# Kernel tuning notes

Measured on AMD Instinct MI355X. Metric: run time of the kernel, lower is better.

## Reference

```python
import jax, jax.numpy as jnp
import numpy as np

B, S, E, H = 8, 2048, 1024, 64  # batch, seq (== block_size), emb_size, head_size


def setup_inputs() -> dict:
    key = jax.random.key(0)
    ks = jax.random.split(key, 7)
    s = 1.0 / np.sqrt(E)  # ~ torch Linear default init scale
    return {
        "x": jax.random.normal(ks[0], (B, S, E), dtype=jnp.float32),
        "Wk": jax.random.uniform(ks[1], (H, E), jnp.float32, -s, s),
        "bk": jax.random.uniform(ks[2], (H,), jnp.float32, -s, s),
        "Wq": jax.random.uniform(ks[3], (H, E), jnp.float32, -s, s),
        "bq": jax.random.uniform(ks[4], (H,), jnp.float32, -s, s),
        "Wv": jax.random.uniform(ks[5], (H, E), jnp.float32, -s, s),
        "bv": jax.random.uniform(ks[6], (H,), jnp.float32, -s, s),
    }


def reference(x, Wk, bk, Wq, bq, Wv, bv):
    # Linear projections (torch Linear: y = x @ W.T + b)
    xk = jnp.einsum('bse,he->bsh', x, Wk) + bk  # [B,S,H]
    xq = jnp.einsum('bse,he->bsh', x, Wq) + bq
    xv = jnp.einsum('bse,he->bsh', x, Wv) + bv
    # raw scores q @ k^T  -> [B,S,S]
    wei = jnp.einsum('bqh,bkh->bqk', xq, xk)
    # causal mask (encoder=True branch in source; tril==0 -> -inf)
    causal = jnp.tril(jnp.ones((x.shape[1], x.shape[1]), dtype=bool))
    wei = jnp.where(causal, wei, -jnp.inf)
    # NOTE: source divides by head_size**(-0.5), i.e. MULTIPLIES by sqrt(head_size)
    scale = jnp.asarray(Wk.shape[0], jnp.float32) ** 0.5
    wei = jax.nn.softmax(wei * scale, axis=-1)
    return jnp.einsum('bqk,bkh->bqh', wei, xv)
```

## Files before the change

kernel.cpp:

```cpp
#include <hip/hip_runtime.h>

typedef _Float16 f16;
typedef _Float16 f16x8 __attribute__((ext_vector_type(8)));
typedef _Float16 f16x4 __attribute__((ext_vector_type(4)));
typedef __fp16 fp16x2 __attribute__((ext_vector_type(2)));
typedef float f32x4 __attribute__((ext_vector_type(4)));

#define MFMA16(a, b, c) __builtin_amdgcn_mfma_f32_16x16x32_f16(a, b, c, 0, 0, 0)

constexpr int Bn = 8, Sn = 2048, En = 1024, Hn = 64;
constexpr int Mn = Bn * Sn;
constexpr float QSCALE = 11.5415603f;
constexpr float THR = 11.5f;

__device__ __forceinline__ void gload_lds16(const void* g, void* lds) {
    __builtin_amdgcn_global_load_lds(
        (const __attribute__((address_space(1))) void*)g,
        (__attribute__((address_space(3))) void*)lds, 16, 0, 0);
}
__device__ __forceinline__ void wait_vm8() {
    asm volatile("s_waitcnt vmcnt(8)" ::: "memory");
    __builtin_amdgcn_sched_barrier(0);
}
__device__ __forceinline__ void wait_vm0() {
    asm volatile("s_waitcnt vmcnt(0)" ::: "memory");
    __builtin_amdgcn_sched_barrier(0);
}
__device__ __forceinline__ void barrier_raw() {
    __builtin_amdgcn_s_barrier();
    __builtin_amdgcn_sched_barrier(0);
}
__device__ __forceinline__ f16x8 cvt8(float4 lo, float4 hi) {
    union { f16x8 v; fp16x2 h[4]; } u;
    u.h[0] = __builtin_amdgcn_cvt_pkrtz(lo.x, lo.y);
    u.h[1] = __builtin_amdgcn_cvt_pkrtz(lo.z, lo.w);
    u.h[2] = __builtin_amdgcn_cvt_pkrtz(hi.x, hi.y);
    u.h[3] = __builtin_amdgcn_cvt_pkrtz(hi.z, hi.w);
    return u.v;
}


__global__ __launch_bounds__(256) void convw_kernel(
    const float* __restrict__ Wq, const float* __restrict__ Wk,
    const float* __restrict__ Wv, f16* __restrict__ Wc)
{
    const int h = blockIdx.x * 256 + threadIdx.x;
    const int kt = h / 1536;
    const int rem = h - kt * 1536;
    const int rr = rem >> 3;
    const int c = rem & 7;
    const int set = rr >> 6;
    const float* src = (set == 0 ? Wq : (set == 1 ? Wk : Wv))
                       + (size_t)(rr & 63) * En + kt * 64 + c * 8;
    float4 v0 = *reinterpret_cast<const float4*>(src);
    float4 v1 = *reinterpret_cast<const float4*>(src + 4);
    f16x8 o = cvt8(v0, v1);
    const int cs = c ^ (rr & 7);
    *reinterpret_cast<f16x8*>(Wc + (size_t)kt * 12288 + rr * 64 + cs * 8) = o;
}

__global__ __launch_bounds__(256) void proj_kernel(
    const float* __restrict__ x, const f16* __restrict__ Wc,
    const float* __restrict__ bq, const float* __restrict__ bk,
    const float* __restrict__ bv,
    f16* __restrict__ qws, f16* __restrict__ kws, f16* __restrict__ vtws)
{
    __shared__ __align__(16) char ldsb[2 * 32768];
    const int tid = threadIdx.x;
    const int w = tid >> 6, l = tid & 63;
    const int l15 = l & 15, lhi = l >> 4;
    const int Mbase = blockIdx.x * 32;

    f32x4 acc[6];
#pragma unroll
    for (int i = 0; i < 6; ++i) acc[i] = (f32x4){0.f, 0.f, 0.f, 0.f};

#define WSTAGE(buf, kb)                                                       \
    {                                                                         \
        const f16* wt_ = Wc + (size_t)(kb) * 12288;                           \
        _Pragma("unroll")                                                     \
        for (int r_ = 0; r_ < 6; ++r_)                                        \
            gload_lds16(wt_ + r_ * 2048 + w * 512 + l * 8,                    \
                        ldsb + (buf) * 32768 + r_ * 4096 + w * 1024);         \
    }

#define XSTAGE(buf, kb)                                                       \
    {                                                                         \
        _Pragma("unroll")                                                     \
        for (int e_ = 0; e_ < 2; ++e_) {                                      \
            const int r_ = e_ * 16 + w * 4 + (l >> 4);                        \
            const float* xs_ = x + (size_t)(Mbase + r_) * En + (kb) * 64      \
                               + (((l & 15) ^ (r_ & 7)) * 4);                 \
            gload_lds16(xs_, ldsb + (buf) * 32768 + 24576                     \
                             + e_ * 4096 + w * 1024);                         \
        }                                                                     \
    }

#define COMPUTE(buf)                                                          \
    {                                                                         \
        f16x8 a_[2][2];                                                       \
        _Pragma("unroll")                                                     \
        for (int sub_ = 0; sub_ < 2; ++sub_) {                                \
            const int xrow_ = sub_ * 16 + l15;                                \
            const char* xb_ = ldsb + (buf) * 32768 + 24576 + xrow_ * 256;     \
            _Pragma("unroll")                                                 \
            for (int kc_ = 0; kc_ < 2; ++kc_) {                               \
                const int c0_ = kc_ * 8 + lhi * 2;                            \
                float4 lo_ = *reinterpret_cast<const float4*>(                \
                    xb_ + ((c0_ ^ (l15 & 7)) * 16));                          \
                float4 hi_ = *reinterpret_cast<const float4*>(                \
                    xb_ + (((c0_ + 1) ^ (l15 & 7)) * 16));                    \
                a_[sub_][kc_] = cvt8(lo_, hi_);                               \
            }                                                                 \
        }                                                                     \
        _Pragma("unroll")                                                     \
        for (int i_ = 0; i_ < 3; ++i_) {                                      \
            const int row16_ = (w * 3 + i_) * 16 + l15;                       \
            _Pragma("unroll")                                                 \
            for (int kc_ = 0; kc_ < 2; ++kc_) {                               \
                const int addr_ = (buf) * 32768 + row16_ * 128                \
                    + ((kc_ * 64 + lhi * 16) ^ ((l15 & 7) << 4));             \
                f16x8 b_ = *reinterpret_cast<const f16x8*>(ldsb + addr_);     \
                acc[i_] = MFMA16(a_[0][kc_], b_, acc[i_]);                    \
                acc[3 + i_] = MFMA16(a_[1][kc_], b_, acc[3 + i_]);            \
            }                                                                 \
        }                                                                     \
    }

    WSTAGE(0, 0);
    XSTAGE(0, 0);
#pragma unroll
    for (int i = 0; i < 16; ++i) {
        const int cur = i & 1;
        if (i < 15) {
            WSTAGE(cur ^ 1, i + 1);
            XSTAGE(cur ^ 1, i + 1);
            wait_vm8();
        } else {
            wait_vm0();
        }
        barrier_raw();
        COMPUTE(cur);
        barrier_raw();
    }
#undef WSTAGE
#undef XSTAGE
#undef COMPUTE

    const int batch = Mbase >> 11;
#pragma unroll
    for (int sub = 0; sub < 2; ++sub) {
        const int r0 = Mbase + sub * 16 + lhi * 4;
#pragma unroll
        for (int i = 0; i < 3; ++i) {
            const int nt = w * 3 + i;
            const int set = nt >> 2;
            const int h = (nt & 3) * 16 + l15;
            const float bias = (set == 0 ? bq : (set == 1 ? bk : bv))[h];
            const f32x4 a = acc[sub * 3 + i];
            if (set < 2) {
                f16* dst = (set == 0) ? qws : kws;
                const float scale = (set == 0) ? QSCALE : 1.0f;
                const int kc = h >> 5;
                const int lhk = (h >> 3) & 3;
                const int j = h & 7;
#pragma unroll
                for (int r = 0; r < 4; ++r) {
                    const int s = (r0 + r) & (Sn - 1);
                    const int t16 = s >> 4;
                    const int l15k = s & 15;
                    dst[(size_t)((batch * 128 + t16) * 2 + kc) * 512
                        + (lhk * 16 + l15k) * 8 + j] =
                        (f16)((a[r] + bias) * scale);
                }
            } else {
                const int s0v = r0 & (Sn - 1);
                const int kt = s0v >> 5;
                const int spl = ((s0v & 12) << 1) + ((s0v & 16) ? 4 : 0);
                const int lhv = spl >> 3;
                const int j0 = spl & 7;
                const int ntv = h >> 4;
                const int l15v = h & 15;
                f16x4 hv = {(f16)(a[0] + bias), (f16)(a[1] + bias),
                            (f16)(a[2] + bias), (f16)(a[3] + bias)};
                *reinterpret_cast<f16x4*>(
                    &vtws[(size_t)((batch * 64 + kt) * 4 + ntv) * 512
                          + (lhv * 16 + l15v) * 8 + j0]) = hv;
            }
        }
    }
}

__global__ __launch_bounds__(256, 3) void attn_kernel(
    const f16* __restrict__ qws, const f16* __restrict__ kws,
    const f16* __restrict__ vtws, float* __restrict__ out,
    float* __restrict__ slots)
{
    const int tid = threadIdx.x;
    const int w = tid >> 6, l = tid & 63;
    const int l15 = l & 15, lhi = l >> 4;

    const int L = blockIdx.x * 4 + w;
    const int u = (int)(((unsigned)L * 997u) % 2304u);
    const int b = u / 288;
    const int t = u - b * 288;
    int k = 0;
#pragma unroll
    for (int gg = 1; gg < 8; ++gg)
        if (t >= 4 * gg * (gg + 1)) k = gg;
    const int rem = t - 4 * k * (k + 1);
    const int jq = rem / (k + 1);
    const int c = rem - jq * (k + 1);
    const int J = 8 * k + jq;

    const int qbase = J * 32;
    const int nkt = J + 1;
    const int ts = c * 8;
    const int te = (ts + 8 < nkt) ? ts + 8 : nkt;
    const bool hasDiag = (te == nkt);
    const int nfull = te - (hasDiag ? 1 : 0);

    f16x8 qf[2][2];
#pragma unroll
    for (int rs = 0; rs < 2; ++rs)
#pragma unroll
        for (int kc = 0; kc < 2; ++kc)
            qf[rs][kc] = *reinterpret_cast<const f16x8*>(
                &qws[(size_t)((b * 128 + J * 2 + rs) * 2 + kc) * 512 + l * 8]);

    f32x4 O[2][4];
#pragma unroll
    for (int rs = 0; rs < 2; ++rs)
#pragma unroll
        for (int nt = 0; nt < 4; ++nt) O[rs][nt] = (f32x4){0.f, 0.f, 0.f, 0.f};
    float m1[2] = {-1e30f, -1e30f}, l1[2] = {0.f, 0.f};

#define ATTN_ITER(KT, MASKED)                                                 \
    {                                                                         \
        f16x8 kf[2][2];                                                       \
        _Pragma("unroll") for (int nt = 0; nt < 2; ++nt)                      \
        _Pragma("unroll") for (int kc = 0; kc < 2; ++kc)                      \
            kf[nt][kc] = *reinterpret_cast<const f16x8*>(                     \
                &kws[(size_t)((b * 128 + (KT) * 2 + nt) * 2 + kc) * 512       \
                     + l * 8]);                                               \
        f32x4 Sv[2][2];                                                       \
        _Pragma("unroll") for (int rs = 0; rs < 2; ++rs)                      \
        _Pragma("unroll") for (int nt = 0; nt < 2; ++nt) {                    \
            f32x4 sa = (f32x4){0.f, 0.f, 0.f, 0.f};                           \
            sa = MFMA16(kf[nt][0], qf[rs][0], sa);                            \
            sa = MFMA16(kf[nt][1], qf[rs][1], sa);                            \
            Sv[rs][nt] = sa;                                                  \
        }                                                                     \
        float tv[2][2][4];                                                    \
        float mx[2];                                                          \
        _Pragma("unroll") for (int rs = 0; rs < 2; ++rs) {                    \
            _Pragma("unroll") for (int nt = 0; nt < 2; ++nt)                  \
            _Pragma("unroll") for (int r = 0; r < 4; ++r) {                   \
                float v = Sv[rs][nt][r];                                      \
                if (MASKED) {                                                 \
                    const int key_ = nt * 16 + lhi * 4 + r;                   \
                    const int qq_ = rs * 16 + l15;                            \
                    v = (key_ <= qq_) ? v : -1e30f;                           \
                }                                                             \
                tv[rs][nt][r] = v;                                            \
            }                                                                 \
            float a0 = fmaxf(fmaxf(tv[rs][0][0], tv[rs][0][1]),               \
                             fmaxf(tv[rs][0][2], tv[rs][0][3]));              \
            float a1 = fmaxf(fmaxf(tv[rs][1][0], tv[rs][1][1]),               \
                             fmaxf(tv[rs][1][2], tv[rs][1][3]));              \
            float m_ = fmaxf(a0, a1);                                         \
            m_ = fmaxf(m_, __shfl_xor(m_, 16));                               \
            m_ = fmaxf(m_, __shfl_xor(m_, 32));                               \
            mx[rs] = m_;                                                      \
        }                                                                     \
        const int need = (mx[0] > m1[0] + THR) || (mx[1] > m1[1] + THR);      \
        if (__any(need)) {                                                    \
            _Pragma("unroll") for (int rs = 0; rs < 2; ++rs) {                \
                const float mn = fmaxf(m1[rs], mx[rs]);                       \
                const float al = exp2f(m1[rs] - mn);                          \
                l1[rs] *= al;                                                 \
                _Pragma("unroll") for (int nt = 0; nt < 4; ++nt)              \
                _Pragma("unroll") for (int r = 0; r < 4; ++r)                 \
                    O[rs][nt][r] *= al;                                       \
                m1[rs] = mn;                                                  \
            }                                                                 \
        }                                                                     \
        f16x8 pa[2];                                                          \
        _Pragma("unroll") for (int rs = 0; rs < 2; ++rs) {                    \
            float p_[8];                                                      \
            float s_ = 0.f;                                                   \
            _Pragma("unroll") for (int nt = 0; nt < 2; ++nt)                  \
            _Pragma("unroll") for (int r = 0; r < 4; ++r) {                   \
                const float e_ = exp2f(tv[rs][nt][r] - m1[rs]);               \
                p_[nt * 4 + r] = e_;                                          \
                s_ += e_;                                                     \
            }                                                                 \
            s_ += __shfl_xor(s_, 16);                                         \
            s_ += __shfl_xor(s_, 32);                                         \
            l1[rs] += s_;                                                     \
            pa[rs] = (f16x8){(f16)p_[0], (f16)p_[1], (f16)p_[2], (f16)p_[3],  \
                             (f16)p_[4], (f16)p_[5], (f16)p_[6], (f16)p_[7]}; \
        }                                                                     \
        _Pragma("unroll") for (int nt = 0; nt < 4; ++nt) {                    \
            f16x8 vf = *reinterpret_cast<const f16x8*>(                       \
                &vtws[(size_t)((b * 64 + (KT)) * 4 + nt) * 512 + l * 8]);     \
            O[0][nt] = MFMA16(vf, pa[0], O[0][nt]);                           \
            O[1][nt] = MFMA16(vf, pa[1], O[1][nt]);                           \
        }                                                                     \
    }

    for (int kt = ts; kt < nfull; ++kt) ATTN_ITER(kt, false);
    if (hasDiag) ATTN_ITER(J, true);
#undef ATTN_ITER

    if (J < 8) {
#pragma unroll
        for (int rs = 0; rs < 2; ++rs) {
            const float inv = 1.0f / l1[rs];
            const size_t ro = ((size_t)b * Sn + qbase + rs * 16 + l15) * Hn;
#pragma unroll
            for (int nt = 0; nt < 4; ++nt) {
                float4 o = {O[rs][nt][0] * inv, O[rs][nt][1] * inv,
                            O[rs][nt][2] * inv, O[rs][nt][3] * inv};
                *reinterpret_cast<float4*>(&out[ro + nt * 16 + lhi * 4]) = o;
            }
        }
    } else {
        float* sl = slots + (size_t)(b * 280 + 4 * k * (k + 1) - 8
                                     + jq * (k + 1) + c) * 1088;
        f16* so = reinterpret_cast<f16*>(sl + 64);
#pragma unroll
        for (int rs = 0; rs < 2; ++rs) {
            const int row = rs * 16 + l15;
            const float inv = 1.0f / l1[rs];
            if (lhi == 0) { sl[row] = m1[rs]; sl[32 + row] = l1[rs]; }
#pragma unroll
            for (int nt = 0; nt < 4; ++nt) {
                f16x4 hv = {(f16)(O[rs][nt][0] * inv), (f16)(O[rs][nt][1] * inv),
                            (f16)(O[rs][nt][2] * inv), (f16)(O[rs][nt][3] * inv)};
                *reinterpret_cast<f16x4*>(
                    &so[row * 64 + nt * 16 + lhi * 4]) = hv;
            }
        }
    }
}

__global__ __launch_bounds__(256) void comb_kernel(
    const float* __restrict__ slots, float* __restrict__ out)
{
    const int id = blockIdx.x;
    const int b = id / 56, jj = id - b * 56;
    const int J = 8 + jj;
    const int k = J >> 3;
    const int nch = k + 1;
    const float* base = slots + (size_t)(b * 280 + 4 * k * (k + 1) - 8
                                         + (J - 8 * k) * (k + 1)) * 1088;
    const int tid = threadIdx.x;
    const int row = tid >> 3;
    const int h0 = (tid & 7) * 8;

    float mg = -1e30f;
    for (int cc = 0; cc < nch; ++cc)
        mg = fmaxf(mg, base[cc * 1088 + row]);
    float den = 0.f;
    float num[8] = {0.f, 0.f, 0.f, 0.f, 0.f, 0.f, 0.f, 0.f};
    for (int cc = 0; cc < nch; ++cc) {
        const float* sl = base + cc * 1088;
        const float wgt = sl[32 + row] * exp2f(sl[row] - mg);
        den += wgt;
        const f16* so = reinterpret_cast<const f16*>(sl + 64);
        f16x8 ov = *reinterpret_cast<const f16x8*>(&so[row * 64 + h0]);
#pragma unroll
        for (int i = 0; i < 8; ++i) num[i] += (float)ov[i] * wgt;
    }
    const float inv = 1.0f / den;
    const size_t ro = ((size_t)b * Sn + J * 32 + row) * Hn + h0;
    float4 o0 = {num[0] * inv, num[1] * inv, num[2] * inv, num[3] * inv};
    float4 o1 = {num[4] * inv, num[5] * inv, num[6] * inv, num[7] * inv};
    *reinterpret_cast<float4*>(&out[ro]) = o0;
    *reinterpret_cast<float4*>(&out[ro + 4]) = o1;
}

extern "C" void kernel_launch(void* const* d_in, const int* in_sizes, int n_in,
                              void* d_out, int out_size, void* d_ws, size_t ws_size,
                              hipStream_t stream) {
    const float* x  = (const float*)d_in[0];
    const float* Wk = (const float*)d_in[1];
    const float* bk = (const float*)d_in[2];
    const float* Wq = (const float*)d_in[3];
    const float* bq = (const float*)d_in[4];
    const float* Wv = (const float*)d_in[5];
    const float* bv = (const float*)d_in[6];

    f16* qws  = (f16*)d_ws;
    f16* kws  = qws + (size_t)Mn * Hn;
    f16* vtws = kws + (size_t)Mn * Hn;
    f16* Wc   = vtws + (size_t)Mn * Hn;
    float* slots = (float*)(Wc + 196608);

    convw_kernel<<<96, 256, 0, stream>>>(Wq, Wk, Wv, Wc);
    proj_kernel<<<512, 256, 0, stream>>>(x, Wc, bq, bk, bv, qws, kws, vtws);
    attn_kernel<<<576, 256, 0, stream>>>(qws, kws, vtws, (float*)d_out, slots);
    comb_kernel<<<448, 256, 0, stream>>>(slots, (float*)d_out);
}
```

Measured before the change: 53.50 us.

## Pre-pack x and weights into MFMA fragment layout, drop LDS staging in projection

Adds a kernel that converts x to fp16 and stores it in per-lane MFMA fragment order in the workspace. The weight conversion kernel is changed to write the same fragment layout. The projection kernel then loads fragments directly from global memory with no LDS double buffering or barriers. The aim is to remove LDS traffic, in-loop conversions and synchronisation, at the cost of an extra kernel and an extra fp16 write and read of all of x.

New measurement: 69.50 us. 1.3x slower.

```diff
diff --git a/kernel.cpp b/kernel.cpp
--- a/kernel.cpp
+++ b/kernel.cpp
@@ -17,10 +17,6 @@
     __builtin_amdgcn_global_load_lds(
         (const __attribute__((address_space(1))) void*)g,
         (__attribute__((address_space(3))) void*)lds, 16, 0, 0);
-}
-__device__ __forceinline__ void wait_vm8() {
-    asm volatile("s_waitcnt vmcnt(8)" ::: "memory");
-    __builtin_amdgcn_sched_barrier(0);
 }
 __device__ __forceinline__ void wait_vm0() {
     asm volatile("s_waitcnt vmcnt(0)" ::: "memory");
@@ -44,108 +40,88 @@
     const float* __restrict__ Wq, const float* __restrict__ Wk,
     const float* __restrict__ Wv, f16* __restrict__ Wc)
 {
-    const int h = blockIdx.x * 256 + threadIdx.x;
-    const int kt = h / 1536;
-    const int rem = h - kt * 1536;
-    const int rr = rem >> 3;
-    const int c = rem & 7;
-    const int set = rr >> 6;
+    const int id = blockIdx.x * 256 + threadIdx.x;
+    const int l = id & 63;
+    const int frag = id >> 6;
+    const int kc = frag & 1;
+    const int kt = (frag >> 1) & 15;
+    const int nt = frag >> 5;
+    const int set = nt >> 2;
     const float* src = (set == 0 ? Wq : (set == 1 ? Wk : Wv))
-                       + (size_t)(rr & 63) * En + kt * 64 + c * 8;
+                       + (size_t)((nt & 3) * 16 + (l & 15)) * En
+                       + kt * 64 + kc * 32 + (l >> 4) * 8;
     float4 v0 = *reinterpret_cast<const float4*>(src);
     float4 v1 = *reinterpret_cast<const float4*>(src + 4);
-    f16x8 o = cvt8(v0, v1);
-    const int cs = c ^ (rr & 7);
-    *reinterpret_cast<f16x8*>(Wc + (size_t)kt * 12288 + rr * 64 + cs * 8) = o;
+    *reinterpret_cast<f16x8*>(Wc + (size_t)frag * 512 + l * 8) = cvt8(v0, v1);
+}
+
+__global__ __launch_bounds__(256) void xrepack_kernel(
+    const float* __restrict__ x, f16* __restrict__ xc)
+{
+    __shared__ __align__(16) char xl[65536];
+    const int tid = threadIdx.x;
+    const int w = tid >> 6, l = tid & 63;
+    const int l15 = l & 15, lhi = l >> 4;
+    const int mtile = blockIdx.x;
+
+#pragma unroll
+    for (int r = 0; r < 16; ++r) {
+        const float* src = x + ((size_t)mtile * 16 + r) * En
+                           + ((tid ^ (r & 7)) * 4);
+        gload_lds16(src, xl + r * 4096 + w * 1024);
+    }
+    wait_vm0();
+    barrier_raw();
+
+#pragma unroll
+    for (int e = 0; e < 8; ++e) {
+        const int f = w * 8 + e;
+        const int cc = (f >> 1) * 16 + (f & 1) * 8 + lhi * 2;
+        const char* rb = xl + l15 * 4096;
+        float4 lo = *reinterpret_cast<const float4*>(
+            rb + ((cc ^ (l15 & 7)) * 16));
+        float4 hi = *reinterpret_cast<const float4*>(
+            rb + (((cc + 1) ^ (l15 & 7)) * 16));
+        *reinterpret_cast<f16x8*>(
+            xc + ((size_t)mtile * 32 + f) * 512 + l * 8) = cvt8(lo, hi);
+    }
 }
 
 __global__ __launch_bounds__(256) void proj_kernel(
-    const float* __restrict__ x, const f16* __restrict__ Wc,
+    const f16* __restrict__ xc, const f16* __restrict__ Wc,
     const float* __restrict__ bq, const float* __restrict__ bk,
     const float* __restrict__ bv,
     f16* __restrict__ qws, f16* __restrict__ kws, f16* __restrict__ vtws)
 {
-    __shared__ __align__(16) char ldsb[2 * 32768];
     const int tid = threadIdx.x;
     const int w = tid >> 6, l = tid & 63;
     const int l15 = l & 15, lhi = l >> 4;
-    const int Mbase = blockIdx.x * 32;
+    const int mp = blockIdx.x;
+    const int Mbase = mp * 32;
 
     f32x4 acc[6];
 #pragma unroll
     for (int i = 0; i < 6; ++i) acc[i] = (f32x4){0.f, 0.f, 0.f, 0.f};
 
-#define WSTAGE(buf, kb)                                                       \
-    {                                                                         \
-        const f16* wt_ = Wc + (size_t)(kb) * 12288;                           \
-        _Pragma("unroll")                                                     \
-        for (int r_ = 0; r_ < 6; ++r_)                                        \
-            gload_lds16(wt_ + r_ * 2048 + w * 512 + l * 8,                    \
-                        ldsb + (buf) * 32768 + r_ * 4096 + w * 1024);         \
-    }
-
-#define XSTAGE(buf, kb)                                                       \
-    {                                                                         \
-        _Pragma("unroll")                                                     \
-        for (int e_ = 0; e_ < 2; ++e_) {                                      \
-            const int r_ = e_ * 16 + w * 4 + (l >> 4);                        \
-            const float* xs_ = x + (size_t)(Mbase + r_) * En + (kb) * 64      \
-                               + (((l & 15) ^ (r_ & 7)) * 4);                 \
-            gload_lds16(xs_, ldsb + (buf) * 32768 + 24576                     \
-                             + e_ * 4096 + w * 1024);                         \
-        }                                                                     \
-    }
-
-#define COMPUTE(buf)                                                          \
-    {                                                                         \
-        f16x8 a_[2][2];                                                       \
-        _Pragma("unroll")                                                     \
-        for (int sub_ = 0; sub_ < 2; ++sub_) {                                \
-            const int xrow_ = sub_ * 16 + l15;                                \
-            const char* xb_ = ldsb + (buf) * 32768 + 24576 + xrow_ * 256;     \
-            _Pragma("unroll")                                                 \
-            for (int kc_ = 0; kc_ < 2; ++kc_) {                               \
-                const int c0_ = kc_ * 8 + lhi * 2;                            \
-                float4 lo_ = *reinterpret_cast<const float4*>(                \
-                    xb_ + ((c0_ ^ (l15 & 7)) * 16));                          \
-                float4 hi_ = *reinterpret_cast<const float4*>(                \
-                    xb_ + (((c0_ + 1) ^ (l15 & 7)) * 16));                    \
-                a_[sub_][kc_] = cvt8(lo_, hi_);                               \
-            }                                                                 \
-        }                                                                     \
-        _Pragma("unroll")                                                     \
-        for (int i_ = 0; i_ < 3; ++i_) {                                      \
-            const int row16_ = (w * 3 + i_) * 16 + l15;                       \
-            _Pragma("unroll")                                                 \
-            for (int kc_ = 0; kc_ < 2; ++kc_) {                               \
-                const int addr_ = (buf) * 32768 + row16_ * 128                \
-                    + ((kc_ * 64 + lhi * 16) ^ ((l15 & 7) << 4));             \
-                f16x8 b_ = *reinterpret_cast<const f16x8*>(ldsb + addr_);     \
-                acc[i_] = MFMA16(a_[0][kc_], b_, acc[i_]);                    \
-                acc[3 + i_] = MFMA16(a_[1][kc_], b_, acc[3 + i_]);            \
-            }                                                                 \
-        }                                                                     \
-    }
-
-    WSTAGE(0, 0);
-    XSTAGE(0, 0);
-#pragma unroll
-    for (int i = 0; i < 16; ++i) {
-        const int cur = i & 1;
-        if (i < 15) {
-            WSTAGE(cur ^ 1, i + 1);
-            XSTAGE(cur ^ 1, i + 1);
-            wait_vm8();
-        } else {
-            wait_vm0();
+#pragma unroll
+    for (int kt = 0; kt < 16; ++kt) {
+#pragma unroll
+        for (int kc = 0; kc < 2; ++kc) {
+            const int fk = kt * 2 + kc;
+            f16x8 xf[2];
+#pragma unroll
+            for (int s = 0; s < 2; ++s)
+                xf[s] = *reinterpret_cast<const f16x8*>(
+                    xc + ((size_t)(mp * 2 + s) * 32 + fk) * 512 + l * 8);
+#pragma unroll
+            for (int i = 0; i < 3; ++i) {
+                f16x8 wf = *reinterpret_cast<const f16x8*>(
+                    Wc + ((size_t)(w * 3 + i) * 32 + fk) * 512 + l * 8);
+                acc[i] = MFMA16(xf[0], wf, acc[i]);
+                acc[3 + i] = MFMA16(xf[1], wf, acc[3 + i]);
+            }
         }
-        barrier_raw();
-        COMPUTE(cur);
-        barrier_raw();
-    }
-#undef WSTAGE
-#undef XSTAGE
-#undef COMPUTE
+    }
 
     const int batch = Mbase >> 11;
 #pragma unroll
@@ -396,10 +372,12 @@
     f16* kws  = qws + (size_t)Mn * Hn;
     f16* vtws = kws + (size_t)Mn * Hn;
     f16* Wc   = vtws + (size_t)Mn * Hn;
-    float* slots = (float*)(Wc + 196608);
+    f16* xc   = Wc + 196608;
+    float* slots = (float*)(xc + (size_t)Mn * En);
 
     convw_kernel<<<96, 256, 0, stream>>>(Wq, Wk, Wv, Wc);
-    proj_kernel<<<512, 256, 0, stream>>>(x, Wc, bq, bk, bv, qws, kws, vtws);
+    xrepack_kernel<<<1024, 256, 0, stream>>>(x, xc);
+    proj_kernel<<<512, 256, 0, stream>>>(xc, Wc, bq, bk, bv, qws, kws, vtws);
     attn_kernel<<<576, 256, 0, stream>>>(qws, kws, vtws, (float*)d_out, slots);
     comb_kernel<<<448, 256, 0, stream>>>(slots, (float*)d_out);
 }
```
